# Performance work log

Measured on AMD Instinct MI355X. Metric: run time of the kernel, lower is better.

The kernel has to match this reference:

```python
import jax, jax.numpy as jnp
import numpy as np

# quantization formats
E_Q, M_Q = 4, 3      # E4M3 fp8 for input/param quantizers
E_A, M_A = 5, 10     # fp16-like accumulate / output format


def quant(x, exp, man):
    """Round-to-nearest-even float quantization to (exp, man) bits,
    with subnormals and saturation (mptorch float_quantize semantics)."""
    ebias = 2 ** (exp - 1) - 1
    emin = 1 - ebias                      # min normal exponent
    maxv = (2.0 - 2.0 ** (-man)) * 2.0 ** ebias
    ax = jnp.abs(x)
    e = jnp.floor(jnp.log2(jnp.where(ax > 0, ax, 1.0)))
    e = jnp.maximum(e, emin)              # subnormal range shares emin scale
    scale = jnp.exp2(man - e)
    q = jnp.round(x * scale) / scale      # jnp.round is half-to-even
    return jnp.clip(q, -maxv, maxv)


def qgemm(x, wt, exp_add, man_add):
    """Custom-precision GEMM x[M,K] @ wt[K,N] with fma=True:
    the running accumulator is requantized to (exp_add, man_add)
    after every rank-1 (per-k) fused multiply-add."""
    M, K = x.shape
    N = wt.shape[1]

    def step(acc, xw):
        xk, wk = xw                       # [M], [N]
        acc = quant(acc + xk[:, None] * wk[None, :], exp_add, man_add)
        return acc, None

    acc0 = jnp.zeros((M, N), x.dtype)
    acc, _ = jax.lax.scan(step, acc0, (x.T, wt))
    return acc


def setup_inputs() -> dict:
    key = jax.random.key(0)
    k1, k2, k3 = jax.random.split(key, 3)
    in_f, out_f, m = 1024, 1024, 2048
    x = jax.random.normal(k1, (m, in_f), jnp.float32)
    weight = jax.random.normal(k2, (out_f, in_f), jnp.float32) / np.float32(np.sqrt(in_f))
    bound = 1.0 / np.float32(np.sqrt(in_f))
    bias = jax.random.uniform(k3, (out_f,), jnp.float32, -bound, bound)
    return {"x": x, "weight": weight, "bias": bias}


def reference(x, weight, bias):
    qx = quant(x, E_Q, M_Q)               # input_quant
    qw = quant(weight, E_Q, M_Q)          # param_quant
    qb = quant(bias, E_Q, M_Q)            # param_quant
    out = qgemm(qx, qw.T, E_A, M_A)       # float_gemm with fma accumulation
    out = out + qb[None, :]
    out = quant(out, E_A, M_A)            # output requantization
    return out
```

## Files before the change

kernel.cpp:

```cpp
#include <hip/hip_runtime.h>
#include <hip/hip_fp16.h>


#define M_DIM 2048
#define N_DIM 1024
#define K_DIM 1024

#define BM 32
#define BN 128
#define BK 64
#define NCHUNK (K_DIM / BK)

typedef unsigned u32;

__device__ __forceinline__ float quant_e4m3(float v) {
  unsigned au = __float_as_uint(v) & 0x7fffffffu;
  if (au == 0u) return v;
  int e = (int)(au >> 23) - 127;
  if (e < -6) e = -6;
  float s  = __uint_as_float((unsigned)(130 - e) << 23);
  float is = __uint_as_float((unsigned)(124 + e) << 23);
  float r = rintf(v * s) * is;
  return fminf(240.f, fmaxf(-240.f, r));
}

__global__ __launch_bounds__(256) void prep_kernel(const float* __restrict__ x,
                                                   const float* __restrict__ w,
                                                   u32* __restrict__ xP,
                                                   u32* __restrict__ wI) {
  __shared__ float tile[32][33];
  const int tx = threadIdx.x & 31;
  const int ty = threadIdx.x >> 5;
  if (blockIdx.x < 2048) {
    const int c0 = (blockIdx.x & 31) * 32;
    const int r0 = (blockIdx.x >> 5) * 32;
#pragma unroll
    for (int i = 0; i < 4; i++) {
      int r = r0 + ty + i * 8;
      tile[ty + i * 8][tx] = quant_e4m3(x[(size_t)r * K_DIM + c0 + tx]);
    }
    __syncthreads();
#pragma unroll
    for (int i = 0; i < 2; i++) {
      int tl = ty + i * 8;
      u32 lo = (u32)__half_as_ushort(__float2half(tile[tx][2 * tl]));
      u32 hi = (u32)__half_as_ushort(__float2half(tile[tx][2 * tl + 1]));
      xP[(size_t)(c0 / 2 + tl) * M_DIM + r0 + tx] = lo | (hi << 16);
    }
  } else {
    const int b = blockIdx.x - 2048;
    const int k0 = (b & 31) * 32;
    const int n0 = (b >> 5) * 32;
#pragma unroll
    for (int i = 0; i < 4; i++) {
      int n = n0 + ty + i * 8;
      tile[ty + i * 8][tx] = quant_e4m3(w[(size_t)n * K_DIM + k0 + tx]);
    }
    __syncthreads();
    if (threadIdx.x < 128) {
      const int tpl = threadIdx.x >> 3;
      const int n4l = threadIdx.x & 7;
      ushort h[8];
#pragma unroll
      for (int j = 0; j < 2; j++)
#pragma unroll
        for (int c = 0; c < 4; c++)
          h[j * 4 + c] = __half_as_ushort(__float2half(tile[n4l * 4 + c][tpl * 2 + j]));
      uint4 o;
      o.x = h[0] | ((u32)h[1] << 16);
      o.y = h[2] | ((u32)h[3] << 16);
      o.z = h[4] | ((u32)h[5] << 16);
      o.w = h[6] | ((u32)h[7] << 16);
      *reinterpret_cast<uint4*>(wI + (size_t)(k0 / 2 + tpl) * N_DIM + n0 + n4l * 4) = o;
    }
  }
}


__device__ __forceinline__ void gld16(const void* g, void* l) {
  __builtin_amdgcn_global_load_lds((const __attribute__((address_space(1))) u32*)g,
                                   (__attribute__((address_space(3))) u32*)l, 16, 0, 0);
}

__device__ __forceinline__ void pkfma_lo(u32& acc, u32 x, u32 w) {
  asm("v_pk_fma_f16 %0, %1, %2, %0 op_sel:[0,0,0] op_sel_hi:[0,1,1]"
      : "+v"(acc) : "v"(x), "v"(w));
}
__device__ __forceinline__ void pkfma_hi(u32& acc, u32 x, u32 w) {
  asm("v_pk_fma_f16 %0, %1, %2, %0 op_sel:[1,0,0] op_sel_hi:[1,1,1]"
      : "+v"(acc) : "v"(x), "v"(w));
}

__global__ __launch_bounds__(256, 2) void gemm_qfma(const u32* __restrict__ xP,
                                                    const u32* __restrict__ wI,
                                                    const float* __restrict__ b,
                                                    float* __restrict__ outp) {
  __shared__ __align__(16) u32 xs[2][BK / 2][BM];
  __shared__ __align__(16) u32 wsh[2][BK / 2][BN];
  const int tid = threadIdx.x;
  const int tn = tid & 31;
  const int tm = tid >> 5;
  const int bn0 = blockIdx.x * BN;
  const int bm0 = blockIdx.y * BM;

  u32 acc[4][2];
#pragma unroll
  for (int i = 0; i < 4; i++) { acc[i][0] = 0u; acc[i][1] = 0u; }

  const u32* wsrc = wI + (size_t)(tid >> 5) * N_DIM + bn0 + ((tid & 31) << 2);
  const u32* xsrc = xP + (size_t)(tid >> 3) * M_DIM + bm0 + ((tid & 7) << 2);

  auto stage = [&](int ch, int buf) {
    const u32* wp = wsrc + (size_t)ch * (BK / 2) * N_DIM;
    char* wl = (char*)&wsh[buf][0][0] + tid * 16;
#pragma unroll
    for (int p = 0; p < 4; p++)
      gld16(wp + (size_t)(p * 8) * N_DIM, wl + p * 4096);
    gld16(xsrc + (size_t)ch * (BK / 2) * M_DIM,
          (char*)&xs[buf][0][0] + tid * 16);
  };

  auto compute = [&](int buf) {
#pragma unroll
    for (int tp = 0; tp < BK / 2; tp++) {
      const uint4 xv = *reinterpret_cast<const uint4*>(&xs[buf][tp][tm << 2]);
      const uint4 wv = *reinterpret_cast<const uint4*>(&wsh[buf][tp][tn << 2]);
      pkfma_lo(acc[0][0], xv.x, wv.x); pkfma_lo(acc[0][1], xv.x, wv.y);
      pkfma_lo(acc[1][0], xv.y, wv.x); pkfma_lo(acc[1][1], xv.y, wv.y);
      pkfma_lo(acc[2][0], xv.z, wv.x); pkfma_lo(acc[2][1], xv.z, wv.y);
      pkfma_lo(acc[3][0], xv.w, wv.x); pkfma_lo(acc[3][1], xv.w, wv.y);
      pkfma_hi(acc[0][0], xv.x, wv.z); pkfma_hi(acc[0][1], xv.x, wv.w);
      pkfma_hi(acc[1][0], xv.y, wv.z); pkfma_hi(acc[1][1], xv.y, wv.w);
      pkfma_hi(acc[2][0], xv.z, wv.z); pkfma_hi(acc[2][1], xv.z, wv.w);
      pkfma_hi(acc[3][0], xv.w, wv.z); pkfma_hi(acc[3][1], xv.w, wv.w);
    }
  };

  stage(0, 0);
  __syncthreads();
#pragma unroll 1
  for (int ch = 0; ch < NCHUNK; ch += 2) {
    stage(ch + 1, 1);
    compute(0);
    __syncthreads();
    if (ch + 2 < NCHUNK) stage(ch + 2, 0);
    compute(1);
    __syncthreads();
  }

  const int nc = bn0 + (tn << 2);
  float4 bq;
  bq.x = quant_e4m3(b[nc + 0]);
  bq.y = quant_e4m3(b[nc + 1]);
  bq.z = quant_e4m3(b[nc + 2]);
  bq.w = quant_e4m3(b[nc + 3]);
#pragma unroll
  for (int i = 0; i < 4; i++) {
    __half2 a0 = *reinterpret_cast<__half2*>(&acc[i][0]);
    __half2 a1 = *reinterpret_cast<__half2*>(&acc[i][1]);
    float4 o;
    o.x = __half2float(__float2half(__low2float(a0)  + bq.x));
    o.y = __half2float(__float2half(__high2float(a0) + bq.y));
    o.z = __half2float(__float2half(__low2float(a1)  + bq.z));
    o.w = __half2float(__float2half(__high2float(a1) + bq.w));
    *reinterpret_cast<float4*>(outp + (size_t)(bm0 + (tm << 2) + i) * N_DIM + nc) = o;
  }
}

extern "C" void kernel_launch(void* const* d_in, const int* in_sizes, int n_in,
                              void* d_out, int out_size, void* d_ws, size_t ws_size,
                              hipStream_t stream) {
  const float* x = (const float*)d_in[0];
  const float* w = (const float*)d_in[1];
  const float* b = (const float*)d_in[2];
  float* outp = (float*)d_out;

  char* ws = (char*)d_ws;
  u32* xP = (u32*)ws;
  u32* wI = (u32*)(ws + (size_t)(4 << 20));

  hipLaunchKernelGGL(prep_kernel, dim3(2048 + 1024), dim3(256), 0, stream,
                     x, w, xP, wI);
  hipLaunchKernelGGL(gemm_qfma, dim3(N_DIM / BN, M_DIM / BM), dim3(256), 0, stream,
                     xP, wI, b, outp);
}
```

Before: 112.4 us.

## Load x per-wave into registers directly and drop x shared-memory staging

Prep now writes x in a wave-blocked layout (8 rows by K/2 pairs) and packs w as n-pairs, so each wave in the GEMM loads its 8 rows of x straight from global memory into registers, double-buffered in register arrays. Only w is staged through LDS. Each lane now computes an 8x2 output tile instead of 4x4. This removes the x LDS traffic and its staging, but raises register pressure (32 uint4 buffers) and relies on global-load latency being hidden by the register double buffering, with broadcast-style loads of x that are the same across lanes.

```diff
diff --git a/kernel.cpp b/kernel.cpp
--- a/kernel.cpp
+++ b/kernel.cpp
@@ -26,8 +26,8 @@
 
 __global__ __launch_bounds__(256) void prep_kernel(const float* __restrict__ x,
                                                    const float* __restrict__ w,
-                                                   u32* __restrict__ xP,
-                                                   u32* __restrict__ wI) {
+                                                   u32* __restrict__ xPw,
+                                                   u32* __restrict__ wP) {
   __shared__ float tile[32][33];
   const int tx = threadIdx.x & 31;
   const int ty = threadIdx.x >> 5;
@@ -45,7 +45,8 @@
       int tl = ty + i * 8;
       u32 lo = (u32)__half_as_ushort(__float2half(tile[tx][2 * tl]));
       u32 hi = (u32)__half_as_ushort(__float2half(tile[tx][2 * tl + 1]));
-      xP[(size_t)(c0 / 2 + tl) * M_DIM + r0 + tx] = lo | (hi << 16);
+      xPw[(size_t)(r0 / 8 + (tx >> 3)) * (K_DIM / 2 * 8) +
+          (c0 / 2 + tl) * 8 + (tx & 7)] = lo | (hi << 16);
     }
   } else {
     const int b = blockIdx.x - 2048;
@@ -57,22 +58,14 @@
       tile[ty + i * 8][tx] = quant_e4m3(w[(size_t)n * K_DIM + k0 + tx]);
     }
     __syncthreads();
-    if (threadIdx.x < 128) {
-      const int tpl = threadIdx.x >> 3;
-      const int n4l = threadIdx.x & 7;
-      ushort h[8];
-#pragma unroll
-      for (int j = 0; j < 2; j++)
-#pragma unroll
-        for (int c = 0; c < 4; c++)
-          h[j * 4 + c] = __half_as_ushort(__float2half(tile[n4l * 4 + c][tpl * 2 + j]));
-      uint4 o;
-      o.x = h[0] | ((u32)h[1] << 16);
-      o.y = h[2] | ((u32)h[3] << 16);
-      o.z = h[4] | ((u32)h[5] << 16);
-      o.w = h[6] | ((u32)h[7] << 16);
-      *reinterpret_cast<uint4*>(wI + (size_t)(k0 / 2 + tpl) * N_DIM + n0 + n4l * 4) = o;
-    }
+    const int tpl = threadIdx.x >> 4;
+    const int npl = threadIdx.x & 15;
+    u32 a0 = (u32)__half_as_ushort(__float2half(tile[2 * npl][2 * tpl])) |
+             ((u32)__half_as_ushort(__float2half(tile[2 * npl + 1][2 * tpl])) << 16);
+    u32 a1 = (u32)__half_as_ushort(__float2half(tile[2 * npl][2 * tpl + 1])) |
+             ((u32)__half_as_ushort(__float2half(tile[2 * npl + 1][2 * tpl + 1])) << 16);
+    uint2 o; o.x = a0; o.y = a1;
+    *reinterpret_cast<uint2*>(wP + (size_t)(k0 / 2 + tpl) * N_DIM + n0 + 2 * npl) = o;
   }
 }
 
@@ -91,79 +84,83 @@
       : "+v"(acc) : "v"(x), "v"(w));
 }
 
-__global__ __launch_bounds__(256, 2) void gemm_qfma(const u32* __restrict__ xP,
-                                                    const u32* __restrict__ wI,
+__global__ __launch_bounds__(256, 2) void gemm_qfma(const u32* __restrict__ xPw,
+                                                    const u32* __restrict__ wP,
                                                     const float* __restrict__ b,
                                                     float* __restrict__ outp) {
-  __shared__ __align__(16) u32 xs[2][BK / 2][BM];
   __shared__ __align__(16) u32 wsh[2][BK / 2][BN];
   const int tid = threadIdx.x;
-  const int tn = tid & 31;
-  const int tm = tid >> 5;
+  const int lane = tid & 63;
+  const int wid = tid >> 6;
   const int bn0 = blockIdx.x * BN;
   const int bm0 = blockIdx.y * BM;
 
-  u32 acc[4][2];
+  u32 acc[8];
 #pragma unroll
-  for (int i = 0; i < 4; i++) { acc[i][0] = 0u; acc[i][1] = 0u; }
+  for (int i = 0; i < 8; i++) acc[i] = 0u;
 
-  const u32* wsrc = wI + (size_t)(tid >> 5) * N_DIM + bn0 + ((tid & 31) << 2);
-  const u32* xsrc = xP + (size_t)(tid >> 3) * M_DIM + bm0 + ((tid & 7) << 2);
+  const u32* wsrc = wP + (size_t)(tid >> 5) * N_DIM + bn0 + ((tid & 31) << 2);
+  char* const wldst = (char*)&wsh[0][0][0] + tid * 16;
 
   auto stage = [&](int ch, int buf) {
     const u32* wp = wsrc + (size_t)ch * (BK / 2) * N_DIM;
-    char* wl = (char*)&wsh[buf][0][0] + tid * 16;
+    char* wl = wldst + buf * (BK / 2) * BN * 4;
 #pragma unroll
     for (int p = 0; p < 4; p++)
       gld16(wp + (size_t)(p * 8) * N_DIM, wl + p * 4096);
-    gld16(xsrc + (size_t)ch * (BK / 2) * M_DIM,
-          (char*)&xs[buf][0][0] + tid * 16);
   };
 
-  auto compute = [&](int buf) {
+  const u32* const xw = xPw + (size_t)(blockIdx.y * 4 + wid) * (K_DIM / 2 * 8);
+
+  uint4 xA[16], xB[16];
+
+#define LOADG(dst, g)                                                   \
+  {                                                                     \
+    const uint4* p_ = reinterpret_cast<const uint4*>(xw + (size_t)(g) * 64); \
+    _Pragma("unroll") for (int i_ = 0; i_ < 16; i_++) dst[i_] = p_[i_]; \
+  }
+
+  auto computeG = [&](const uint4 (&xb)[16], int buf, int gc) {
 #pragma unroll
-    for (int tp = 0; tp < BK / 2; tp++) {
-      const uint4 xv = *reinterpret_cast<const uint4*>(&xs[buf][tp][tm << 2]);
-      const uint4 wv = *reinterpret_cast<const uint4*>(&wsh[buf][tp][tn << 2]);
-      pkfma_lo(acc[0][0], xv.x, wv.x); pkfma_lo(acc[0][1], xv.x, wv.y);
-      pkfma_lo(acc[1][0], xv.y, wv.x); pkfma_lo(acc[1][1], xv.y, wv.y);
-      pkfma_lo(acc[2][0], xv.z, wv.x); pkfma_lo(acc[2][1], xv.z, wv.y);
-      pkfma_lo(acc[3][0], xv.w, wv.x); pkfma_lo(acc[3][1], xv.w, wv.y);
-      pkfma_hi(acc[0][0], xv.x, wv.z); pkfma_hi(acc[0][1], xv.x, wv.w);
-      pkfma_hi(acc[1][0], xv.y, wv.z); pkfma_hi(acc[1][1], xv.y, wv.w);
-      pkfma_hi(acc[2][0], xv.z, wv.z); pkfma_hi(acc[2][1], xv.z, wv.w);
-      pkfma_hi(acc[3][0], xv.w, wv.z); pkfma_hi(acc[3][1], xv.w, wv.w);
+    for (int j = 0; j < 8; j++) {
+      const uint2 wv = *reinterpret_cast<const uint2*>(&wsh[buf][gc * 8 + j][lane << 1]);
+      const uint4 xl = xb[2 * j];
+      const uint4 xh = xb[2 * j + 1];
+      pkfma_lo(acc[0], xl.x, wv.x); pkfma_lo(acc[1], xl.y, wv.x);
+      pkfma_lo(acc[2], xl.z, wv.x); pkfma_lo(acc[3], xl.w, wv.x);
+      pkfma_lo(acc[4], xh.x, wv.x); pkfma_lo(acc[5], xh.y, wv.x);
+      pkfma_lo(acc[6], xh.z, wv.x); pkfma_lo(acc[7], xh.w, wv.x);
+      pkfma_hi(acc[0], xl.x, wv.y); pkfma_hi(acc[1], xl.y, wv.y);
+      pkfma_hi(acc[2], xl.z, wv.y); pkfma_hi(acc[3], xl.w, wv.y);
+      pkfma_hi(acc[4], xh.x, wv.y); pkfma_hi(acc[5], xh.y, wv.y);
+      pkfma_hi(acc[6], xh.z, wv.y); pkfma_hi(acc[7], xh.w, wv.y);
     }
   };
 
   stage(0, 0);
+  LOADG(xA, 0);
   __syncthreads();
 #pragma unroll 1
-  for (int ch = 0; ch < NCHUNK; ch += 2) {
-    stage(ch + 1, 1);
-    compute(0);
-    __syncthreads();
-    if (ch + 2 < NCHUNK) stage(ch + 2, 0);
-    compute(1);
+  for (int ch = 0; ch < NCHUNK; ch++) {
+    if (ch + 1 < NCHUNK) stage(ch + 1, (ch + 1) & 1);
+    const int g0 = ch * 4;
+    LOADG(xB, g0 + 1); computeG(xA, ch & 1, 0);
+    LOADG(xA, g0 + 2); computeG(xB, ch & 1, 1);
+    LOADG(xB, g0 + 3); computeG(xA, ch & 1, 2);
+    LOADG(xA, g0 + 4); computeG(xB, ch & 1, 3);
     __syncthreads();
   }
 
-  const int nc = bn0 + (tn << 2);
-  float4 bq;
-  bq.x = quant_e4m3(b[nc + 0]);
-  bq.y = quant_e4m3(b[nc + 1]);
-  bq.z = quant_e4m3(b[nc + 2]);
-  bq.w = quant_e4m3(b[nc + 3]);
+  const int nc = bn0 + (lane << 1);
+  const float bq0 = quant_e4m3(b[nc]);
+  const float bq1 = quant_e4m3(b[nc + 1]);
 #pragma unroll
-  for (int i = 0; i < 4; i++) {
-    __half2 a0 = *reinterpret_cast<__half2*>(&acc[i][0]);
-    __half2 a1 = *reinterpret_cast<__half2*>(&acc[i][1]);
-    float4 o;
-    o.x = __half2float(__float2half(__low2float(a0)  + bq.x));
-    o.y = __half2float(__float2half(__high2float(a0) + bq.y));
-    o.z = __half2float(__float2half(__low2float(a1)  + bq.z));
-    o.w = __half2float(__float2half(__high2float(a1) + bq.w));
-    *reinterpret_cast<float4*>(outp + (size_t)(bm0 + (tm << 2) + i) * N_DIM + nc) = o;
+  for (int i = 0; i < 8; i++) {
+    __half2 a = *reinterpret_cast<__half2*>(&acc[i]);
+    float2 o;
+    o.x = __half2float(__float2half(__low2float(a)  + bq0));
+    o.y = __half2float(__float2half(__high2float(a) + bq1));
+    *reinterpret_cast<float2*>(outp + (size_t)(bm0 + (wid << 3) + i) * N_DIM + nc) = o;
   }
 }
 
@@ -176,11 +173,11 @@
   float* outp = (float*)d_out;
 
   char* ws = (char*)d_ws;
-  u32* xP = (u32*)ws;
-  u32* wI = (u32*)(ws + (size_t)(4 << 20));
+  u32* xPw = (u32*)ws;
+  u32* wP = (u32*)(ws + (size_t)(4 << 20));
 
   hipLaunchKernelGGL(prep_kernel, dim3(2048 + 1024), dim3(256), 0, stream,
-                     x, w, xP, wI);
+                     x, w, xPw, wP);
   hipLaunchKernelGGL(gemm_qfma, dim3(N_DIM / BN, M_DIM / BM), dim3(256), 0, stream,
-                     xP, wI, b, outp);
+                     xPw, wP, b, outp);
 }
```

New measurement: 136.2 us. 1.21x slower.

## Switch GEMM to square 64x64 tiles with 2x2 wave layout and pair-interleaved weights

Applied to the files above, without the earlier changes.

Changes the block tile from 32x128 to 64x64 and arranges the four waves in a 2x2 grid, each computing a 32x32 sub-tile. The weight staging layout changes from 4-column interleaved packing to adjacent-n pairs per k-pair, and the prep kernel now writes it with all 256 threads. The square tile evens out the global bytes loaded per block between x and w and changes the LDS read pattern per wave. The grid shape changes, so occupancy and L2 reuse behaviour shift as well.

```diff
diff --git a/kernel.cpp b/kernel.cpp
--- a/kernel.cpp
+++ b/kernel.cpp
@@ -6,8 +6,8 @@
 #define N_DIM 1024
 #define K_DIM 1024
 
-#define BM 32
-#define BN 128
+#define BM 64
+#define BN 64
 #define BK 64
 #define NCHUNK (K_DIM / BK)
 
@@ -27,7 +27,7 @@
 __global__ __launch_bounds__(256) void prep_kernel(const float* __restrict__ x,
                                                    const float* __restrict__ w,
                                                    u32* __restrict__ xP,
-                                                   u32* __restrict__ wI) {
+                                                   u32* __restrict__ wP) {
   __shared__ float tile[32][33];
   const int tx = threadIdx.x & 31;
   const int ty = threadIdx.x >> 5;
@@ -57,22 +57,14 @@
       tile[ty + i * 8][tx] = quant_e4m3(w[(size_t)n * K_DIM + k0 + tx]);
     }
     __syncthreads();
-    if (threadIdx.x < 128) {
-      const int tpl = threadIdx.x >> 3;
-      const int n4l = threadIdx.x & 7;
-      ushort h[8];
-#pragma unroll
-      for (int j = 0; j < 2; j++)
-#pragma unroll
-        for (int c = 0; c < 4; c++)
-          h[j * 4 + c] = __half_as_ushort(__float2half(tile[n4l * 4 + c][tpl * 2 + j]));
-      uint4 o;
-      o.x = h[0] | ((u32)h[1] << 16);
-      o.y = h[2] | ((u32)h[3] << 16);
-      o.z = h[4] | ((u32)h[5] << 16);
-      o.w = h[6] | ((u32)h[7] << 16);
-      *reinterpret_cast<uint4*>(wI + (size_t)(k0 / 2 + tpl) * N_DIM + n0 + n4l * 4) = o;
-    }
+    const int tpl = threadIdx.x >> 4;
+    const int npl = threadIdx.x & 15;
+    u32 a0 = (u32)__half_as_ushort(__float2half(tile[2 * npl][2 * tpl])) |
+             ((u32)__half_as_ushort(__float2half(tile[2 * npl + 1][2 * tpl])) << 16);
+    u32 a1 = (u32)__half_as_ushort(__float2half(tile[2 * npl][2 * tpl + 1])) |
+             ((u32)__half_as_ushort(__float2half(tile[2 * npl + 1][2 * tpl + 1])) << 16);
+    uint2 o; o.x = a0; o.y = a1;
+    *reinterpret_cast<uint2*>(wP + (size_t)(k0 / 2 + tpl) * N_DIM + n0 + 2 * npl) = o;
   }
 }
 
@@ -92,47 +84,56 @@
 }
 
 __global__ __launch_bounds__(256, 2) void gemm_qfma(const u32* __restrict__ xP,
-                                                    const u32* __restrict__ wI,
+                                                    const u32* __restrict__ wP,
                                                     const float* __restrict__ b,
                                                     float* __restrict__ outp) {
   __shared__ __align__(16) u32 xs[2][BK / 2][BM];
-  __shared__ __align__(16) u32 wsh[2][BK / 2][BN];
+  __shared__ __align__(16) u32 ws[2][BK / 2][BN];
   const int tid = threadIdx.x;
-  const int tn = tid & 31;
-  const int tm = tid >> 5;
+  const int lane = tid & 63;
+  const int wv = tid >> 6;
+  const int wr = wv >> 1;
+  const int wc = wv & 1;
+  const int tml = lane >> 3;
+  const int tnl = lane & 7;
   const int bn0 = blockIdx.x * BN;
   const int bm0 = blockIdx.y * BM;
+  const int xoff = wr * 32 + tml * 4;
+  const int woff = wc * 32 + tnl * 4;
 
   u32 acc[4][2];
 #pragma unroll
   for (int i = 0; i < 4; i++) { acc[i][0] = 0u; acc[i][1] = 0u; }
 
-  const u32* wsrc = wI + (size_t)(tid >> 5) * N_DIM + bn0 + ((tid & 31) << 2);
-  const u32* xsrc = xP + (size_t)(tid >> 3) * M_DIM + bm0 + ((tid & 7) << 2);
+  const int srow = tid >> 4;
+  const int scol = (tid & 15) << 2;
+  const u32* xsrc = xP + (size_t)srow * M_DIM + bm0 + scol;
+  const u32* wsrc = wP + (size_t)srow * N_DIM + bn0 + scol;
 
   auto stage = [&](int ch, int buf) {
+    const u32* xp = xsrc + (size_t)ch * (BK / 2) * M_DIM;
     const u32* wp = wsrc + (size_t)ch * (BK / 2) * N_DIM;
-    char* wl = (char*)&wsh[buf][0][0] + tid * 16;
-#pragma unroll
-    for (int p = 0; p < 4; p++)
-      gld16(wp + (size_t)(p * 8) * N_DIM, wl + p * 4096);
-    gld16(xsrc + (size_t)ch * (BK / 2) * M_DIM,
-          (char*)&xs[buf][0][0] + tid * 16);
+    char* xl = (char*)&xs[buf][0][0] + tid * 16;
+    char* wl = (char*)&ws[buf][0][0] + tid * 16;
+    gld16(xp, xl);
+    gld16(xp + (size_t)16 * M_DIM, xl + 4096);
+    gld16(wp, wl);
+    gld16(wp + (size_t)16 * N_DIM, wl + 4096);
   };
 
   auto compute = [&](int buf) {
 #pragma unroll
     for (int tp = 0; tp < BK / 2; tp++) {
-      const uint4 xv = *reinterpret_cast<const uint4*>(&xs[buf][tp][tm << 2]);
-      const uint4 wv = *reinterpret_cast<const uint4*>(&wsh[buf][tp][tn << 2]);
-      pkfma_lo(acc[0][0], xv.x, wv.x); pkfma_lo(acc[0][1], xv.x, wv.y);
-      pkfma_lo(acc[1][0], xv.y, wv.x); pkfma_lo(acc[1][1], xv.y, wv.y);
-      pkfma_lo(acc[2][0], xv.z, wv.x); pkfma_lo(acc[2][1], xv.z, wv.y);
-      pkfma_lo(acc[3][0], xv.w, wv.x); pkfma_lo(acc[3][1], xv.w, wv.y);
-      pkfma_hi(acc[0][0], xv.x, wv.z); pkfma_hi(acc[0][1], xv.x, wv.w);
-      pkfma_hi(acc[1][0], xv.y, wv.z); pkfma_hi(acc[1][1], xv.y, wv.w);
-      pkfma_hi(acc[2][0], xv.z, wv.z); pkfma_hi(acc[2][1], xv.z, wv.w);
-      pkfma_hi(acc[3][0], xv.w, wv.z); pkfma_hi(acc[3][1], xv.w, wv.w);
+      const uint4 xv = *reinterpret_cast<const uint4*>(&xs[buf][tp][xoff]);
+      const uint4 wv4 = *reinterpret_cast<const uint4*>(&ws[buf][tp][woff]);
+      pkfma_lo(acc[0][0], xv.x, wv4.x); pkfma_lo(acc[0][1], xv.x, wv4.z);
+      pkfma_lo(acc[1][0], xv.y, wv4.x); pkfma_lo(acc[1][1], xv.y, wv4.z);
+      pkfma_lo(acc[2][0], xv.z, wv4.x); pkfma_lo(acc[2][1], xv.z, wv4.z);
+      pkfma_lo(acc[3][0], xv.w, wv4.x); pkfma_lo(acc[3][1], xv.w, wv4.z);
+      pkfma_hi(acc[0][0], xv.x, wv4.y); pkfma_hi(acc[0][1], xv.x, wv4.w);
+      pkfma_hi(acc[1][0], xv.y, wv4.y); pkfma_hi(acc[1][1], xv.y, wv4.w);
+      pkfma_hi(acc[2][0], xv.z, wv4.y); pkfma_hi(acc[2][1], xv.z, wv4.w);
+      pkfma_hi(acc[3][0], xv.w, wv4.y); pkfma_hi(acc[3][1], xv.w, wv4.w);
     }
   };
 
@@ -148,7 +149,7 @@
     __syncthreads();
   }
 
-  const int nc = bn0 + (tn << 2);
+  const int nc = bn0 + wc * 32 + tnl * 4;
   float4 bq;
   bq.x = quant_e4m3(b[nc + 0]);
   bq.y = quant_e4m3(b[nc + 1]);
@@ -163,7 +164,8 @@
     o.y = __half2float(__float2half(__high2float(a0) + bq.y));
     o.z = __half2float(__float2half(__low2float(a1)  + bq.z));
     o.w = __half2float(__float2half(__high2float(a1) + bq.w));
-    *reinterpret_cast<float4*>(outp + (size_t)(bm0 + (tm << 2) + i) * N_DIM + nc) = o;
+    *reinterpret_cast<float4*>(
+        outp + (size_t)(bm0 + wr * 32 + tml * 4 + i) * N_DIM + nc) = o;
   }
 }
 
@@ -175,12 +177,12 @@
   const float* b = (const float*)d_in[2];
   float* outp = (float*)d_out;
 
-  char* ws = (char*)d_ws;
-  u32* xP = (u32*)ws;
-  u32* wI = (u32*)(ws + (size_t)(4 << 20));
+  char* ws_ = (char*)d_ws;
+  u32* xP = (u32*)ws_;
+  u32* wP = (u32*)(ws_ + (size_t)(4 << 20));
 
   hipLaunchKernelGGL(prep_kernel, dim3(2048 + 1024), dim3(256), 0, stream,
-                     x, w, xP, wI);
+                     x, w, xP, wP);
   hipLaunchKernelGGL(gemm_qfma, dim3(N_DIM / BN, M_DIM / BM), dim3(256), 0, stream,
-                     xP, wI, b, outp);
+                     xP, wP, b, outp);
 }
```

After: 110.3 us. Within noise of the previous version (-1.9%).

## Store quantized operands as packed fp8 and convert to fp16 in GEMM inner loop

Applied to the files above, without the earlier changes.

The prep kernel now encodes the E4M3-quantized x and weight as packed fp8 bytes rather than fp16 pairs, halving the intermediate buffer size and the global/LDS traffic per K chunk. The GEMM loads fp8 tiles with fewer global_load_lds calls and converts them to packed fp16 in registers via cvt_pk_f32_fp8 followed by cvt_pkrtz before the same packed FMA accumulation. This adds conversion ALU work to the inner loop, which may outweigh the bandwidth savings in a kernel whose inner loop is dominated by FMA instructions.

```diff
diff --git a/kernel.cpp b/kernel.cpp
--- a/kernel.cpp
+++ b/kernel.cpp
@@ -12,6 +12,7 @@
 #define NCHUNK (K_DIM / BK)
 
 typedef unsigned u32;
+typedef float f32x2 __attribute__((ext_vector_type(2)));
 
 __device__ __forceinline__ float quant_e4m3(float v) {
   unsigned au = __float_as_uint(v) & 0x7fffffffu;
@@ -24,10 +25,21 @@
   return fminf(240.f, fmaxf(-240.f, r));
 }
 
+__device__ __forceinline__ u32 enc_e4m3(float v) {
+  unsigned au = __float_as_uint(v);
+  unsigned sg = (au >> 24) & 0x80u;
+  unsigned a = au & 0x7fffffffu;
+  if (a == 0u) return sg;
+  int e = (int)(a >> 23) - 127;
+  unsigned man = (a >> 20) & 7u;
+  if (e >= -6) return sg | ((unsigned)(e + 7) << 3) | man;
+  return sg | ((8u | man) >> (-6 - e));
+}
+
 __global__ __launch_bounds__(256) void prep_kernel(const float* __restrict__ x,
                                                    const float* __restrict__ w,
-                                                   u32* __restrict__ xP,
-                                                   u32* __restrict__ wI) {
+                                                   u32* __restrict__ xB,
+                                                   u32* __restrict__ wB) {
   __shared__ float tile[32][33];
   const int tx = threadIdx.x & 31;
   const int ty = threadIdx.x >> 5;
@@ -40,39 +52,33 @@
       tile[ty + i * 8][tx] = quant_e4m3(x[(size_t)r * K_DIM + c0 + tx]);
     }
     __syncthreads();
-#pragma unroll
-    for (int i = 0; i < 2; i++) {
-      int tl = ty + i * 8;
-      u32 lo = (u32)__half_as_ushort(__float2half(tile[tx][2 * tl]));
-      u32 hi = (u32)__half_as_ushort(__float2half(tile[tx][2 * tl + 1]));
-      xP[(size_t)(c0 / 2 + tl) * M_DIM + r0 + tx] = lo | (hi << 16);
-    }
+    const int ml = tx;
+    const int ql = ty;
+    u32 v = enc_e4m3(tile[ml][4 * ql + 0])
+          | (enc_e4m3(tile[ml][4 * ql + 1]) << 8)
+          | (enc_e4m3(tile[ml][4 * ql + 2]) << 16)
+          | (enc_e4m3(tile[ml][4 * ql + 3]) << 24);
+    xB[(size_t)(c0 / 4 + ql) * M_DIM + r0 + ml] = v;
   } else {
     const int b = blockIdx.x - 2048;
-    const int k0 = (b & 31) * 32;
-    const int n0 = (b >> 5) * 32;
+    const int k0t = (b & 31) * 32;
+    const int n0t = (b >> 5) * 32;
 #pragma unroll
     for (int i = 0; i < 4; i++) {
-      int n = n0 + ty + i * 8;
-      tile[ty + i * 8][tx] = quant_e4m3(w[(size_t)n * K_DIM + k0 + tx]);
-    }
-    __syncthreads();
-    if (threadIdx.x < 128) {
-      const int tpl = threadIdx.x >> 3;
-      const int n4l = threadIdx.x & 7;
-      ushort h[8];
-#pragma unroll
-      for (int j = 0; j < 2; j++)
-#pragma unroll
-        for (int c = 0; c < 4; c++)
-          h[j * 4 + c] = __half_as_ushort(__float2half(tile[n4l * 4 + c][tpl * 2 + j]));
-      uint4 o;
-      o.x = h[0] | ((u32)h[1] << 16);
-      o.y = h[2] | ((u32)h[3] << 16);
-      o.z = h[4] | ((u32)h[5] << 16);
-      o.w = h[6] | ((u32)h[7] << 16);
-      *reinterpret_cast<uint4*>(wI + (size_t)(k0 / 2 + tpl) * N_DIM + n0 + n4l * 4) = o;
-    }
+      int n = n0t + ty + i * 8;
+      tile[ty + i * 8][tx] = quant_e4m3(w[(size_t)n * K_DIM + k0t + tx]);
+    }
+    __syncthreads();
+    const int u = threadIdx.x & 3;
+    const int cl = (threadIdx.x >> 2) & 7;
+    const int ql = (threadIdx.x >> 5) & 7;
+    const int nl = 4 * cl + 2 * (u & 1);
+    const int kl = 4 * ql + 2 * (u >> 1);
+    u32 v = enc_e4m3(tile[nl][kl])
+          | (enc_e4m3(tile[nl + 1][kl]) << 8)
+          | (enc_e4m3(tile[nl][kl + 1]) << 16)
+          | (enc_e4m3(tile[nl + 1][kl + 1]) << 24);
+    wB[(size_t)(k0t / 4 + ql) * N_DIM + n0t + (cl << 2) + u] = v;
   }
 }
 
@@ -82,6 +88,14 @@
                                    (__attribute__((address_space(3))) u32*)l, 16, 0, 0);
 }
 
+template <int HI>
+__device__ __forceinline__ u32 fp8x2_h2(u32 v) {
+  f32x2 f = __builtin_amdgcn_cvt_pk_f32_fp8((int)v, HI);
+  u32 r;
+  asm("v_cvt_pkrtz_f16_f32 %0, %1, %2" : "=v"(r) : "v"(f[0]), "v"(f[1]));
+  return r;
+}
+
 __device__ __forceinline__ void pkfma_lo(u32& acc, u32 x, u32 w) {
   asm("v_pk_fma_f16 %0, %1, %2, %0 op_sel:[0,0,0] op_sel_hi:[0,1,1]"
       : "+v"(acc) : "v"(x), "v"(w));
@@ -91,12 +105,12 @@
       : "+v"(acc) : "v"(x), "v"(w));
 }
 
-__global__ __launch_bounds__(256, 2) void gemm_qfma(const u32* __restrict__ xP,
-                                                    const u32* __restrict__ wI,
+__global__ __launch_bounds__(256, 2) void gemm_qfma(const u32* __restrict__ xB,
+                                                    const u32* __restrict__ wB,
                                                     const float* __restrict__ b,
                                                     float* __restrict__ outp) {
-  __shared__ __align__(16) u32 xs[2][BK / 2][BM];
-  __shared__ __align__(16) u32 wsh[2][BK / 2][BN];
+  __shared__ __align__(16) u32 xs[2][BK / 4][BM];
+  __shared__ __align__(16) u32 wsu[2][BK / 4][BN];
   const int tid = threadIdx.x;
   const int tn = tid & 31;
   const int tm = tid >> 5;
@@ -107,32 +121,56 @@
 #pragma unroll
   for (int i = 0; i < 4; i++) { acc[i][0] = 0u; acc[i][1] = 0u; }
 
-  const u32* wsrc = wI + (size_t)(tid >> 5) * N_DIM + bn0 + ((tid & 31) << 2);
-  const u32* xsrc = xP + (size_t)(tid >> 3) * M_DIM + bm0 + ((tid & 7) << 2);
+  const u32* xsrc = xB + (size_t)(tid >> 3) * M_DIM + bm0 + ((tid & 7) << 2);
+  const u32* wsrc = wB + (size_t)(tid >> 5) * N_DIM + bn0 + ((tid & 31) << 2);
 
   auto stage = [&](int ch, int buf) {
-    const u32* wp = wsrc + (size_t)ch * (BK / 2) * N_DIM;
-    char* wl = (char*)&wsh[buf][0][0] + tid * 16;
-#pragma unroll
-    for (int p = 0; p < 4; p++)
-      gld16(wp + (size_t)(p * 8) * N_DIM, wl + p * 4096);
-    gld16(xsrc + (size_t)ch * (BK / 2) * M_DIM,
-          (char*)&xs[buf][0][0] + tid * 16);
+    if (tid < 128) {
+      gld16(xsrc + (size_t)ch * (BK / 4) * M_DIM, (char*)&xs[buf][0][0] + tid * 16);
+    }
+    const u32* wp = wsrc + (size_t)ch * (BK / 4) * N_DIM;
+    char* wl = (char*)&wsu[buf][0][0] + tid * 16;
+    gld16(wp, wl);
+    gld16(wp + (size_t)8 * N_DIM, wl + 4096);
   };
 
   auto compute = [&](int buf) {
 #pragma unroll
-    for (int tp = 0; tp < BK / 2; tp++) {
-      const uint4 xv = *reinterpret_cast<const uint4*>(&xs[buf][tp][tm << 2]);
-      const uint4 wv = *reinterpret_cast<const uint4*>(&wsh[buf][tp][tn << 2]);
-      pkfma_lo(acc[0][0], xv.x, wv.x); pkfma_lo(acc[0][1], xv.x, wv.y);
-      pkfma_lo(acc[1][0], xv.y, wv.x); pkfma_lo(acc[1][1], xv.y, wv.y);
-      pkfma_lo(acc[2][0], xv.z, wv.x); pkfma_lo(acc[2][1], xv.z, wv.y);
-      pkfma_lo(acc[3][0], xv.w, wv.x); pkfma_lo(acc[3][1], xv.w, wv.y);
-      pkfma_hi(acc[0][0], xv.x, wv.z); pkfma_hi(acc[0][1], xv.x, wv.w);
-      pkfma_hi(acc[1][0], xv.y, wv.z); pkfma_hi(acc[1][1], xv.y, wv.w);
-      pkfma_hi(acc[2][0], xv.z, wv.z); pkfma_hi(acc[2][1], xv.z, wv.w);
-      pkfma_hi(acc[3][0], xv.w, wv.z); pkfma_hi(acc[3][1], xv.w, wv.w);
+    for (int q = 0; q < BK / 4; q++) {
+      const uint4 xq = *reinterpret_cast<const uint4*>(&xs[buf][q][tm << 2]);
+      const uint4 wq = *reinterpret_cast<const uint4*>(&wsu[buf][q][tn << 2]);
+      {
+        const u32 x0 = fp8x2_h2<0>(xq.x), x1 = fp8x2_h2<0>(xq.y);
+        const u32 x2 = fp8x2_h2<0>(xq.z), x3 = fp8x2_h2<0>(xq.w);
+        const u32 wk0a = fp8x2_h2<0>(wq.x);
+        const u32 wk1a = fp8x2_h2<1>(wq.x);
+        const u32 wk0b = fp8x2_h2<0>(wq.y);
+        const u32 wk1b = fp8x2_h2<1>(wq.y);
+        pkfma_lo(acc[0][0], x0, wk0a); pkfma_lo(acc[0][1], x0, wk0b);
+        pkfma_lo(acc[1][0], x1, wk0a); pkfma_lo(acc[1][1], x1, wk0b);
+        pkfma_lo(acc[2][0], x2, wk0a); pkfma_lo(acc[2][1], x2, wk0b);
+        pkfma_lo(acc[3][0], x3, wk0a); pkfma_lo(acc[3][1], x3, wk0b);
+        pkfma_hi(acc[0][0], x0, wk1a); pkfma_hi(acc[0][1], x0, wk1b);
+        pkfma_hi(acc[1][0], x1, wk1a); pkfma_hi(acc[1][1], x1, wk1b);
+        pkfma_hi(acc[2][0], x2, wk1a); pkfma_hi(acc[2][1], x2, wk1b);
+        pkfma_hi(acc[3][0], x3, wk1a); pkfma_hi(acc[3][1], x3, wk1b);
+      }
+      {
+        const u32 x0 = fp8x2_h2<1>(xq.x), x1 = fp8x2_h2<1>(xq.y);
+        const u32 x2 = fp8x2_h2<1>(xq.z), x3 = fp8x2_h2<1>(xq.w);
+        const u32 wk2a = fp8x2_h2<0>(wq.z);
+        const u32 wk3a = fp8x2_h2<1>(wq.z);
+        const u32 wk2b = fp8x2_h2<0>(wq.w);
+        const u32 wk3b = fp8x2_h2<1>(wq.w);
+        pkfma_lo(acc[0][0], x0, wk2a); pkfma_lo(acc[0][1], x0, wk2b);
+        pkfma_lo(acc[1][0], x1, wk2a); pkfma_lo(acc[1][1], x1, wk2b);
+        pkfma_lo(acc[2][0], x2, wk2a); pkfma_lo(acc[2][1], x2, wk2b);
+        pkfma_lo(acc[3][0], x3, wk2a); pkfma_lo(acc[3][1], x3, wk2b);
+        pkfma_hi(acc[0][0], x0, wk3a); pkfma_hi(acc[0][1], x0, wk3b);
+        pkfma_hi(acc[1][0], x1, wk3a); pkfma_hi(acc[1][1], x1, wk3b);
+        pkfma_hi(acc[2][0], x2, wk3a); pkfma_hi(acc[2][1], x2, wk3b);
+        pkfma_hi(acc[3][0], x3, wk3a); pkfma_hi(acc[3][1], x3, wk3b);
+      }
     }
   };
 
@@ -163,7 +201,8 @@
     o.y = __half2float(__float2half(__high2float(a0) + bq.y));
     o.z = __half2float(__float2half(__low2float(a1)  + bq.z));
     o.w = __half2float(__float2half(__high2float(a1) + bq.w));
-    *reinterpret_cast<float4*>(outp + (size_t)(bm0 + (tm << 2) + i) * N_DIM + nc) = o;
+    *reinterpret_cast<float4*>(
+        outp + (size_t)(bm0 + (tm << 2) + i) * N_DIM + nc) = o;
   }
 }
 
@@ -175,12 +214,12 @@
   const float* b = (const float*)d_in[2];
   float* outp = (float*)d_out;
 
-  char* ws = (char*)d_ws;
-  u32* xP = (u32*)ws;
-  u32* wI = (u32*)(ws + (size_t)(4 << 20));
+  char* ws_ = (char*)d_ws;
+  u32* xB = (u32*)ws_;
+  u32* wB = (u32*)(ws_ + (size_t)(2 << 20));
 
   hipLaunchKernelGGL(prep_kernel, dim3(2048 + 1024), dim3(256), 0, stream,
-                     x, w, xP, wI);
+                     x, w, xB, wB);
   hipLaunchKernelGGL(gemm_qfma, dim3(N_DIM / BN, M_DIM / BM), dim3(256), 0, stream,
-                     xP, wI, b, outp);
-}
+                     xB, wB, b, outp);
+}
```

Result: slower. 136.6 us (+21.6%).
